# Performance work log

Measured on AMD Instinct MI355X. Metric: run time of the kernel, lower is better.

Reference implementation:

```python
import jax, jax.numpy as jnp
import numpy as np

B, C, H, W = 8, 256, 48, 48


def setup_inputs() -> dict:
    key = jax.random.key(0)
    ks = jax.random.split(key, 16)
    d = {
        "rgb": jax.random.normal(ks[0], (B, C, H, W), dtype=jnp.float32),
        "t": jax.random.normal(ks[1], (B, C, H, W), dtype=jnp.float32),
    }
    names = ["wq1", "bq1", "wk1", "bk1", "wv1", "bv1",
             "wq2", "bq2", "wk2", "bk2", "wv2", "bv2"]
    for i, n in enumerate(names):
        if n.startswith("w"):
            d[n] = jax.random.normal(ks[2 + i], (C, C), dtype=jnp.float32) * 0.02
        else:
            d[n] = jax.random.normal(ks[2 + i], (C,), dtype=jnp.float32) * 0.02
    return d


def _cross_attention(x, y, wq, bq, wk, bk, wv, bv):
    # x, y: [b, c, h, w]; 1x1 convs == channel matmuls (ratio=1)
    b, c, h, w = x.shape
    xf = x.reshape(b, c, h * w)  # [b, c, n]
    yf = y.reshape(b, c, h * w)
    q = jnp.einsum('oi,bin->bno', wq, xf) + bq            # [b, n, c]
    k = jnp.einsum('oi,bin->bon', wk, yf) + bk[None, :, None]  # [b, c, n]
    v = jnp.einsum('oi,bin->bno', wv, yf) + bv            # [b, n, c]
    # unscaled attention, exactly as the torch module (no 1/sqrt(c))
    attn = jax.nn.softmax(jnp.einsum('bnc,bcm->bnm', q, k), axis=-1)  # [b, n, n]
    feat = q + jnp.einsum('bnm,bmc->bnc', attn, v)        # residual on q
    return feat.transpose(0, 2, 1).reshape(b, c, h, w)


def reference(rgb, t, wq1, bq1, wk1, bk1, wv1, bv1,
              wq2, bq2, wk2, bk2, wv2, bv2):
    feat_1 = _cross_attention(rgb, t, wq1, bq1, wk1, bk1, wv1, bv1)
    feat_2 = _cross_attention(t, rgb, wq2, bq2, wk2, bk2, wv2, bv2)
    out1 = rgb + feat_1
    out2 = t + feat_2
    return (out1, out2)
```

## Files before the change

kernel.cpp:

```cpp
#include <hip/hip_runtime.h>
#include <hip/hip_bf16.h>
#include <cstdint>

#define B_ 8
#define C_ 256
#define N_ 2304
#define XT_BYTES ((size_t)B_ * N_ * C_ * 2)
#define QK_BYTES ((size_t)16 * N_ * C_ * 2)
#define V_BYTES  ((size_t)16 * C_ * N_ * 2)

typedef __bf16 bf16x8 __attribute__((ext_vector_type(8)));
typedef float  f32x4  __attribute__((ext_vector_type(4)));
static_assert(sizeof(bf16x8) == 16, "");

__global__ __launch_bounds__(256) void k_transpose(
    const float* __restrict__ rgb, const float* __restrict__ tin,
    char* __restrict__ xT)
{
  const int nt = blockIdx.x;
  const int it = blockIdx.y;
  const int z  = blockIdx.z;
  const int src = z >> 3, b = z & 7;
  const float* __restrict__ in = (src ? tin : rgb) + (size_t)b * C_ * N_;
  char* __restrict__ out = xT + (size_t)src * XT_BYTES + (size_t)b * N_ * 512;
  const int i0 = it * 64, n0 = nt * 64;
  __shared__ float raw[64 * 65];
  const int t = threadIdx.x;
  const int rr = t >> 4;
  const int cc = t & 15;
#pragma unroll
  for (int j = 0; j < 4; ++j) {
    const int ii = rr + 16 * j;
    const float4 v = *(const float4*)(in + (size_t)(i0 + ii) * N_ + n0 + cc * 4);
    float* rp = &raw[ii * 65 + cc * 4];
    rp[0] = v.x; rp[1] = v.y; rp[2] = v.z; rp[3] = v.w;
  }
  __syncthreads();
#pragma unroll
  for (int k = 0; k < 4; ++k) {
    const int nl = rr + 16 * k;
    const int n = n0 + nl;
    union { __bf16 h[4]; uint2 u; } pk;
#pragma unroll
    for (int e = 0; e < 4; ++e)
      pk.h[e] = (__bf16)raw[(cc * 4 + e) * 65 + nl];
    const int cb = ((i0 + cc * 4) * 2) ^ ((n & 7) << 4);
    *(uint2*)(out + (size_t)n * 512 + cb) = pk.u;
  }
}

__global__ __launch_bounds__(256) void k_wcvt(
    const float* __restrict__ w0, const float* __restrict__ w1,
    const float* __restrict__ w2, const float* __restrict__ w3,
    const float* __restrict__ w4, const float* __restrict__ w5,
    char* __restrict__ Wb)
{
  const int widx = blockIdx.y;
  const float* w = widx == 0 ? w0 : widx == 1 ? w1 : widx == 2 ? w2
                 : widx == 3 ? w3 : widx == 4 ? w4 : w5;
  const int t = threadIdx.x;
  const int row = blockIdx.x * 8 + (t >> 5);
  const int c8 = (t & 31) * 8;
  const float4 v0 = *(const float4*)(w + row * 256 + c8);
  const float4 v1 = *(const float4*)(w + row * 256 + c8 + 4);
  union { __bf16 h[8]; uint4 u; } pk;
  pk.h[0] = (__bf16)v0.x; pk.h[1] = (__bf16)v0.y; pk.h[2] = (__bf16)v0.z; pk.h[3] = (__bf16)v0.w;
  pk.h[4] = (__bf16)v1.x; pk.h[5] = (__bf16)v1.y; pk.h[6] = (__bf16)v1.z; pk.h[7] = (__bf16)v1.w;
  const int cb = (c8 * 2) ^ ((row & 7) << 4);
  *(uint4*)(Wb + (size_t)(widx * 256 + row) * 512 + cb) = pk.u;
}

__global__ __launch_bounds__(256, 2) void k_proj_qk(
    const char* __restrict__ xT, const char* __restrict__ Wb,
    const float* __restrict__ bq1, const float* __restrict__ bk1,
    const float* __restrict__ bq2, const float* __restrict__ bk2,
    char* __restrict__ Qw, char* __restrict__ Kw)
{
  const int z = blockIdx.z;
  const int b = blockIdx.y;
  const int ntile = blockIdx.x >> 2, otile = blockIdx.x & 3;
  const int n0 = ntile * 128, o0 = otile * 64;
  const int srcT = (z == 1 || z == 2);
  const char* __restrict__ xp = xT + (size_t)srcT * XT_BYTES + (size_t)b * N_ * 512;
  const char* __restrict__ Wp = Wb + (size_t)z * C_ * 512;
  const float* __restrict__ bias = z == 0 ? bq1 : z == 1 ? bk1 : z == 2 ? bq2 : bk2;
  char* __restrict__ outp = ((z == 0 || z == 2) ? Qw : Kw)
                            + (size_t)((z >= 2 ? 8 : 0) + b) * N_ * 512;

  __shared__ alignas(16) char Alds[128 * 128];
  __shared__ alignas(16) char Wlds[64 * 128];
  const int t = threadIdx.x, lane = t & 63, wid = t >> 6;
  const int wm = wid >> 1, wn = wid & 1;
  const int lr = lane & 15, lk = lane >> 4;
  f32x4 acc[4][2] = {};

  for (int ko = 0; ko < 4; ++ko) {
    const int ib = ko * 128;
    __syncthreads();
#pragma unroll
    for (int s = 0; s < 4; ++s) {
      const int flat = s * 4096 + t * 16;
      *(uint4*)(Alds + flat) =
          *(const uint4*)(xp + (size_t)(n0 + (flat >> 7)) * 512 + ib + (flat & 127));
    }
#pragma unroll
    for (int s = 0; s < 2; ++s) {
      const int flat = s * 4096 + t * 16;
      *(uint4*)(Wlds + flat) =
          *(const uint4*)(Wp + (size_t)(o0 + (flat >> 7)) * 512 + ib + (flat & 127));
    }
    __syncthreads();
#pragma unroll
    for (int ks = 0; ks < 2; ++ks) {
      bf16x8 af[4], bfr[2];
#pragma unroll
      for (int mf = 0; mf < 4; ++mf) {
        const int row = wm * 64 + mf * 16 + lr;
        af[mf] = *(const bf16x8*)(Alds + row * 128 + ((ks * 64 + lk * 16) ^ ((row & 7) << 4)));
      }
#pragma unroll
      for (int nf = 0; nf < 2; ++nf) {
        const int row = wn * 32 + nf * 16 + lr;
        bfr[nf] = *(const bf16x8*)(Wlds + row * 128 + ((ks * 64 + lk * 16) ^ ((row & 7) << 4)));
      }
#pragma unroll
      for (int mf = 0; mf < 4; ++mf)
#pragma unroll
        for (int nf = 0; nf < 2; ++nf)
          acc[mf][nf] = __builtin_amdgcn_mfma_f32_16x16x32_bf16(af[mf], bfr[nf], acc[mf][nf], 0, 0, 0);
    }
  }
#pragma unroll
  for (int nf = 0; nf < 2; ++nf) {
    const int c = o0 + wn * 32 + nf * 16 + lr;
    const float bv = bias[c];
#pragma unroll
    for (int mf = 0; mf < 4; ++mf)
#pragma unroll
      for (int r = 0; r < 4; ++r) {
        const int n = n0 + wm * 64 + mf * 16 + lk * 4 + r;
        *(__bf16*)(outp + (size_t)n * 512 + ((c * 2) ^ ((n & 7) << 4))) =
            (__bf16)(acc[mf][nf][r] + bv);
      }
  }
}

__global__ __launch_bounds__(256, 2) void k_proj_v(
    const char* __restrict__ xT, const char* __restrict__ Wb,
    const float* __restrict__ bv1, const float* __restrict__ bv2,
    char* __restrict__ Vw)
{
  const int z = blockIdx.z;
  const int b = blockIdx.y;
  const int ntile = blockIdx.x >> 2, otile = blockIdx.x & 3;
  const int n0 = ntile * 128, o0 = otile * 64;
  const char* __restrict__ xp = xT + (size_t)(z == 0 ? 1 : 0) * XT_BYTES + (size_t)b * N_ * 512;
  const char* __restrict__ Wp = Wb + (size_t)(4 + z) * C_ * 512;
  const float* __restrict__ bias = z ? bv2 : bv1;
  char* __restrict__ outp = Vw + (size_t)(z * 8 + b) * C_ * 4608;

  __shared__ alignas(16) char Xlds[128 * 128];
  __shared__ alignas(16) char Wlds[64 * 128];
  const int t = threadIdx.x, lane = t & 63, wid = t >> 6;
  const int wm = wid >> 1, wn = wid & 1;
  const int lr = lane & 15, lk = lane >> 4;
  f32x4 acc[2][4] = {};

  for (int ko = 0; ko < 4; ++ko) {
    const int ib = ko * 128;
    __syncthreads();
#pragma unroll
    for (int s = 0; s < 4; ++s) {
      const int flat = s * 4096 + t * 16;
      *(uint4*)(Xlds + flat) =
          *(const uint4*)(xp + (size_t)(n0 + (flat >> 7)) * 512 + ib + (flat & 127));
    }
#pragma unroll
    for (int s = 0; s < 2; ++s) {
      const int flat = s * 4096 + t * 16;
      *(uint4*)(Wlds + flat) =
          *(const uint4*)(Wp + (size_t)(o0 + (flat >> 7)) * 512 + ib + (flat & 127));
    }
    __syncthreads();
#pragma unroll
    for (int ks = 0; ks < 2; ++ks) {
      bf16x8 af[2], bfr[4];
#pragma unroll
      for (int mf = 0; mf < 2; ++mf) {
        const int row = wm * 32 + mf * 16 + lr;
        af[mf] = *(const bf16x8*)(Wlds + row * 128 + ((ks * 64 + lk * 16) ^ ((row & 7) << 4)));
      }
#pragma unroll
      for (int nf = 0; nf < 4; ++nf) {
        const int row = wn * 64 + nf * 16 + lr;
        bfr[nf] = *(const bf16x8*)(Xlds + row * 128 + ((ks * 64 + lk * 16) ^ ((row & 7) << 4)));
      }
#pragma unroll
      for (int mf = 0; mf < 2; ++mf)
#pragma unroll
        for (int nf = 0; nf < 4; ++nf)
          acc[mf][nf] = __builtin_amdgcn_mfma_f32_16x16x32_bf16(af[mf], bfr[nf], acc[mf][nf], 0, 0, 0);
    }
  }
#pragma unroll
  for (int mf = 0; mf < 2; ++mf)
#pragma unroll
    for (int r = 0; r < 4; ++r) {
      const int o = o0 + wm * 32 + mf * 16 + lk * 4 + r;
      const float bv = bias[o];
#pragma unroll
      for (int nf = 0; nf < 4; ++nf) {
        const int n = n0 + wn * 64 + nf * 16 + lr;
        *(__bf16*)(outp + (size_t)o * 4608 + ((n * 2) ^ ((o & 7) << 4))) =
            (__bf16)(acc[mf][nf][r] + bv);
      }
    }
}

__global__ __launch_bounds__(256, 2) void k_flash(
    const char* __restrict__ Qw, const char* __restrict__ Kw, const char* __restrict__ Vw,
    const float* __restrict__ rgb, const float* __restrict__ tin,
    float* __restrict__ outp)
{
  const int qt = blockIdx.x;
  const int pair = blockIdx.y;
  const int a = pair >> 3, b = pair & 7;
  const char* __restrict__ Qp = Qw + (size_t)pair * N_ * 512;
  const char* __restrict__ Kp = Kw + (size_t)pair * N_ * 512;
  const char* __restrict__ Vp = Vw + (size_t)pair * C_ * 4608;
  const float* __restrict__ xsrc = (a ? tin : rgb) + (size_t)b * C_ * N_;
  float* __restrict__ op = outp + (size_t)(a * 8 + b) * C_ * N_;

  __shared__ alignas(16) char Klds[64 * 512];
  __shared__ alignas(16) char Vlds[256 * 128];
  __shared__ alignas(16) char Plds[4 * 2048];

  const int t = threadIdx.x, lane = t & 63, w = t >> 6;
  const int lr = lane & 15, lk = lane >> 4;
  const int q0 = qt * 64;

  bf16x8 qf[8];
  {
    const int n = q0 + w * 16 + lr;
    const char* qrow = Qp + (size_t)n * 512;
    const int sw = (n & 7) << 4;
#pragma unroll
    for (int ks = 0; ks < 8; ++ks)
      qf[ks] = *(const bf16x8*)(qrow + ((ks * 64 + lk * 16) ^ sw));
  }

  f32x4 oacc[16] = {};
  float m_run[4], l_run[4];
#pragma unroll
  for (int r = 0; r < 4; ++r) { m_run[r] = -1e30f; l_run[r] = 0.f; }

  for (int kv = 0; kv < 36; ++kv) {
    const size_t kb = (size_t)kv * 64;
    {
      const char* Ksrc = Kp + kb * 512;
#pragma unroll
      for (int s = 0; s < 8; ++s) {
        const int flat = s * 4096 + t * 16;
        *(uint4*)(Klds + flat) = *(const uint4*)(Ksrc + flat);
      }
      const char* Vsrc = Vp + kb * 2;
#pragma unroll
      for (int s = 0; s < 8; ++s) {
        const int flat = s * 4096 + t * 16;
        *(uint4*)(Vlds + flat) =
            *(const uint4*)(Vsrc + (size_t)(flat >> 7) * 4608 + (flat & 127));
      }
    }
    __syncthreads();

    f32x4 s4[4] = {};
#pragma unroll
    for (int mf = 0; mf < 4; ++mf) {
      const int row = mf * 16 + lr;
      const char* kr = Klds + row * 512;
      const int sw = (row & 7) << 4;
#pragma unroll
      for (int ks = 0; ks < 8; ++ks) {
        const bf16x8 kf = *(const bf16x8*)(kr + ((ks * 64 + lk * 16) ^ sw));
        s4[mf] = __builtin_amdgcn_mfma_f32_16x16x32_bf16(qf[ks], kf, s4[mf], 0, 0, 0);
      }
    }

    float scale[4];
#pragma unroll
    for (int r = 0; r < 4; ++r) {
      float m0 = fmaxf(fmaxf(s4[0][r], s4[1][r]), fmaxf(s4[2][r], s4[3][r]));
      m0 = fmaxf(m0, __shfl_xor(m0, 1));
      m0 = fmaxf(m0, __shfl_xor(m0, 2));
      m0 = fmaxf(m0, __shfl_xor(m0, 4));
      m0 = fmaxf(m0, __shfl_xor(m0, 8));
      const float mn = fmaxf(m_run[r], m0);
      scale[r] = __expf(m_run[r] - mn);
      m_run[r] = mn;
    }

    float psum[4] = {0.f, 0.f, 0.f, 0.f};
    char* pw = Plds + w * 2048;
#pragma unroll
    for (int mf = 0; mf < 4; ++mf)
#pragma unroll
      for (int r = 0; r < 4; ++r) {
        const float p = __expf(s4[mf][r] - m_run[r]);
        psum[r] += p;
        const int row = lk * 4 + r;
        const int col = mf * 16 + lr;
        *(__bf16*)(pw + row * 128 + ((col * 2) ^ ((row & 7) << 4))) = (__bf16)p;
      }
#pragma unroll
    for (int r = 0; r < 4; ++r) {
      float s0 = psum[r];
      s0 += __shfl_xor(s0, 1);
      s0 += __shfl_xor(s0, 2);
      s0 += __shfl_xor(s0, 4);
      s0 += __shfl_xor(s0, 8);
      l_run[r] = l_run[r] * scale[r] + s0;
    }
#pragma unroll
    for (int cf = 0; cf < 16; ++cf)
#pragma unroll
      for (int r = 0; r < 4; ++r) oacc[cf][r] *= scale[r];

#pragma unroll
    for (int ks2 = 0; ks2 < 2; ++ks2) {
      const bf16x8 pf =
          *(const bf16x8*)(pw + lr * 128 + ((ks2 * 64 + lk * 16) ^ ((lr & 7) << 4)));
#pragma unroll
      for (int cf = 0; cf < 16; ++cf) {
        const int vr = cf * 16 + lr;
        const bf16x8 vf =
            *(const bf16x8*)(Vlds + vr * 128 + ((ks2 * 64 + lk * 16) ^ ((vr & 7) << 4)));
        oacc[cf] = __builtin_amdgcn_mfma_f32_16x16x32_bf16(pf, vf, oacc[cf], 0, 0, 0);
      }
    }
    __syncthreads();
  }

  float inv[4];
#pragma unroll
  for (int r = 0; r < 4; ++r) inv[r] = 1.0f / l_run[r];
  const int nb = q0 + w * 16 + lk * 4;
#pragma unroll
  for (int cf = 0; cf < 16; ++cf) {
    const int c = cf * 16 + lr;
    const float4 xv = *(const float4*)(xsrc + (size_t)c * N_ + nb);
    float vals[4];
#pragma unroll
    for (int r = 0; r < 4; ++r) {
      const int n = nb + r;
      const float qv =
          (float)(*(const __bf16*)(Qp + (size_t)n * 512 + ((c * 2) ^ ((n & 7) << 4))));
      vals[r] = oacc[cf][r] * inv[r] + qv;
    }
    float4 ov;
    ov.x = vals[0] + xv.x; ov.y = vals[1] + xv.y;
    ov.z = vals[2] + xv.z; ov.w = vals[3] + xv.w;
    *(float4*)(op + (size_t)c * N_ + nb) = ov;
  }
}

extern "C" void kernel_launch(void* const* d_in, const int* in_sizes, int n_in,
                              void* d_out, int out_size, void* d_ws, size_t ws_size,
                              hipStream_t stream) {
  const float* rgb = (const float*)d_in[0];
  const float* tin = (const float*)d_in[1];
  const float* wq1 = (const float*)d_in[2];
  const float* bq1 = (const float*)d_in[3];
  const float* wk1 = (const float*)d_in[4];
  const float* bk1 = (const float*)d_in[5];
  const float* wv1 = (const float*)d_in[6];
  const float* bv1 = (const float*)d_in[7];
  const float* wq2 = (const float*)d_in[8];
  const float* bq2 = (const float*)d_in[9];
  const float* wk2 = (const float*)d_in[10];
  const float* bk2 = (const float*)d_in[11];
  const float* wv2 = (const float*)d_in[12];
  const float* bv2 = (const float*)d_in[13];

  char* ws = (char*)d_ws;
  char* xT = ws;
  char* Qw = ws + 2 * XT_BYTES;
  char* Kw = Qw + QK_BYTES;
  char* Vw = Kw + QK_BYTES;
  char* Wb = Vw + V_BYTES;

  k_transpose<<<dim3(36, 4, 16), 256, 0, stream>>>(rgb, tin, xT);
  k_wcvt<<<dim3(32, 6), 256, 0, stream>>>(wq1, wk1, wq2, wk2, wv1, wv2, Wb);
  k_proj_qk<<<dim3(72, 8, 4), 256, 0, stream>>>(xT, Wb, bq1, bk1, bq2, bk2, Qw, Kw);
  k_proj_v<<<dim3(72, 8, 2), 256, 0, stream>>>(xT, Wb, bv1, bv2, Vw);
  k_flash<<<dim3(36, 16), 256, 0, stream>>>(Qw, Kw, Vw, rgb, tin, (float*)d_out);
}
```

Baseline: 288.5 us.

## Restructure flash kernel: 128-row Q tiles, async LDS loads, lazy softmax rescale

```diff
diff --git a/kernel.cpp b/kernel.cpp
--- a/kernel.cpp
+++ b/kernel.cpp
@@ -12,6 +12,15 @@
 typedef __bf16 bf16x8 __attribute__((ext_vector_type(8)));
 typedef float  f32x4  __attribute__((ext_vector_type(4)));
 static_assert(sizeof(bf16x8) == 16, "");
+
+__device__ __forceinline__ void gload16(const void* g, void* l) {
+  __builtin_amdgcn_global_load_lds(
+      reinterpret_cast<const __attribute__((address_space(1))) uint32_t*>(
+          reinterpret_cast<uintptr_t>(g)),
+      reinterpret_cast<__attribute__((address_space(3))) uint32_t*>(
+          reinterpret_cast<uintptr_t>(l)),
+      16, 0, 0);
+}
 
 __global__ __launch_bounds__(256) void k_transpose(
     const float* __restrict__ rgb, const float* __restrict__ tin,
@@ -212,12 +221,12 @@
       for (int nf = 0; nf < 4; ++nf) {
         const int n = n0 + wn * 64 + nf * 16 + lr;
         *(__bf16*)(outp + (size_t)o * 4608 + ((n * 2) ^ ((o & 7) << 4))) =
-            (__bf16)(acc[mf][nf][r] + bv);
-      }
-    }
-}
-
-__global__ __launch_bounds__(256, 2) void k_flash(
+            (__bf16)(acc[nf == nf ? mf : mf][nf][r] + bv);
+      }
+    }
+}
+
+__global__ __launch_bounds__(256, 2) void k_flash2(
     const char* __restrict__ Qw, const char* __restrict__ Kw, const char* __restrict__ Vw,
     const float* __restrict__ rgb, const float* __restrict__ tin,
     float* __restrict__ outp)
@@ -231,49 +240,47 @@
   const float* __restrict__ xsrc = (a ? tin : rgb) + (size_t)b * C_ * N_;
   float* __restrict__ op = outp + (size_t)(a * 8 + b) * C_ * N_;
 
-  __shared__ alignas(16) char Klds[64 * 512];
-  __shared__ alignas(16) char Vlds[256 * 128];
-  __shared__ alignas(16) char Plds[4 * 2048];
+  __shared__ alignas(16) char smem[81920];
+  char* Klds = smem;
+  char* Vlds = smem + 32768;
+  char* Plds = smem + 65536;
 
   const int t = threadIdx.x, lane = t & 63, w = t >> 6;
   const int lr = lane & 15, lk = lane >> 4;
-  const int q0 = qt * 64;
-
-  bf16x8 qf[8];
-  {
-    const int n = q0 + w * 16 + lr;
+  const int q0 = qt * 128;
+
+  bf16x8 qf[2][8];
+#pragma unroll
+  for (int qs = 0; qs < 2; ++qs) {
+    const int n = q0 + w * 32 + qs * 16 + lr;
     const char* qrow = Qp + (size_t)n * 512;
     const int sw = (n & 7) << 4;
 #pragma unroll
     for (int ks = 0; ks < 8; ++ks)
-      qf[ks] = *(const bf16x8*)(qrow + ((ks * 64 + lk * 16) ^ sw));
-  }
-
-  f32x4 oacc[16] = {};
-  float m_run[4], l_run[4];
-#pragma unroll
-  for (int r = 0; r < 4; ++r) { m_run[r] = -1e30f; l_run[r] = 0.f; }
+      qf[qs][ks] = *(const bf16x8*)(qrow + ((ks * 64 + lk * 16) ^ sw));
+  }
+
+  f32x4 oacc[2][16] = {};
+  float m_run[2][4], l_run[2][4];
+#pragma unroll
+  for (int qs = 0; qs < 2; ++qs)
+#pragma unroll
+    for (int r = 0; r < 4; ++r) { m_run[qs][r] = -1e30f; l_run[qs][r] = 0.f; }
+
+  {
+#pragma unroll
+    for (int s = 0; s < 8; ++s) {
+      const int flat = s * 4096 + t * 16;
+      gload16(Kp + flat, Klds + flat);
+      gload16(Vp + (size_t)(flat >> 7) * 4608 + (flat & 127), Vlds + flat);
+    }
+  }
 
   for (int kv = 0; kv < 36; ++kv) {
-    const size_t kb = (size_t)kv * 64;
-    {
-      const char* Ksrc = Kp + kb * 512;
-#pragma unroll
-      for (int s = 0; s < 8; ++s) {
-        const int flat = s * 4096 + t * 16;
-        *(uint4*)(Klds + flat) = *(const uint4*)(Ksrc + flat);
-      }
-      const char* Vsrc = Vp + kb * 2;
-#pragma unroll
-      for (int s = 0; s < 8; ++s) {
-        const int flat = s * 4096 + t * 16;
-        *(uint4*)(Vlds + flat) =
-            *(const uint4*)(Vsrc + (size_t)(flat >> 7) * 4608 + (flat & 127));
-      }
-    }
-    __syncthreads();
-
-    f32x4 s4[4] = {};
+    __syncthreads();
+
+    f32x4 s4[2][4] = {};
+    __builtin_amdgcn_s_setprio(1);
 #pragma unroll
     for (int mf = 0; mf < 4; ++mf) {
       const int row = mf * 16 + lr;
@@ -282,84 +289,147 @@
 #pragma unroll
       for (int ks = 0; ks < 8; ++ks) {
         const bf16x8 kf = *(const bf16x8*)(kr + ((ks * 64 + lk * 16) ^ sw));
-        s4[mf] = __builtin_amdgcn_mfma_f32_16x16x32_bf16(qf[ks], kf, s4[mf], 0, 0, 0);
-      }
-    }
-
-    float scale[4];
-#pragma unroll
-    for (int r = 0; r < 4; ++r) {
-      float m0 = fmaxf(fmaxf(s4[0][r], s4[1][r]), fmaxf(s4[2][r], s4[3][r]));
-      m0 = fmaxf(m0, __shfl_xor(m0, 1));
-      m0 = fmaxf(m0, __shfl_xor(m0, 2));
-      m0 = fmaxf(m0, __shfl_xor(m0, 4));
-      m0 = fmaxf(m0, __shfl_xor(m0, 8));
-      const float mn = fmaxf(m_run[r], m0);
-      scale[r] = __expf(m_run[r] - mn);
-      m_run[r] = mn;
-    }
-
-    float psum[4] = {0.f, 0.f, 0.f, 0.f};
-    char* pw = Plds + w * 2048;
-#pragma unroll
-    for (int mf = 0; mf < 4; ++mf)
+        s4[0][mf] = __builtin_amdgcn_mfma_f32_16x16x32_bf16(qf[0][ks], kf, s4[0][mf], 0, 0, 0);
+        s4[1][mf] = __builtin_amdgcn_mfma_f32_16x16x32_bf16(qf[1][ks], kf, s4[1][mf], 0, 0, 0);
+      }
+    }
+    __builtin_amdgcn_s_setprio(0);
+    __syncthreads();
+    if (kv + 1 < 36) {
+      const char* Ksrc = Kp + (size_t)(kv + 1) * 64 * 512;
+#pragma unroll
+      for (int s = 0; s < 8; ++s) {
+        const int flat = s * 4096 + t * 16;
+        gload16(Ksrc + flat, Klds + flat);
+      }
+    }
+
+    float pmax[2][4];
+#pragma unroll
+    for (int qs = 0; qs < 2; ++qs)
 #pragma unroll
       for (int r = 0; r < 4; ++r) {
-        const float p = __expf(s4[mf][r] - m_run[r]);
-        psum[r] += p;
-        const int row = lk * 4 + r;
-        const int col = mf * 16 + lr;
-        *(__bf16*)(pw + row * 128 + ((col * 2) ^ ((row & 7) << 4))) = (__bf16)p;
-      }
-#pragma unroll
-    for (int r = 0; r < 4; ++r) {
-      float s0 = psum[r];
-      s0 += __shfl_xor(s0, 1);
-      s0 += __shfl_xor(s0, 2);
-      s0 += __shfl_xor(s0, 4);
-      s0 += __shfl_xor(s0, 8);
-      l_run[r] = l_run[r] * scale[r] + s0;
-    }
-#pragma unroll
-    for (int cf = 0; cf < 16; ++cf)
-#pragma unroll
-      for (int r = 0; r < 4; ++r) oacc[cf][r] *= scale[r];
-
+        float m0 = fmaxf(fmaxf(s4[qs][0][r], s4[qs][1][r]),
+                         fmaxf(s4[qs][2][r], s4[qs][3][r]));
+        m0 = fmaxf(m0, __shfl_xor(m0, 1));
+        m0 = fmaxf(m0, __shfl_xor(m0, 2));
+        m0 = fmaxf(m0, __shfl_xor(m0, 4));
+        m0 = fmaxf(m0, __shfl_xor(m0, 8));
+        pmax[qs][r] = m0;
+      }
+    bool need = false;
+#pragma unroll
+    for (int qs = 0; qs < 2; ++qs)
+#pragma unroll
+      for (int r = 0; r < 4; ++r)
+        need |= (pmax[qs][r] > m_run[qs][r] + 8.f);
+    if (__any(need)) {
+#pragma unroll
+      for (int qs = 0; qs < 2; ++qs)
+#pragma unroll
+        for (int r = 0; r < 4; ++r) {
+          const float mn = fmaxf(m_run[qs][r], pmax[qs][r]);
+          const float sc = __expf(m_run[qs][r] - mn);
+          m_run[qs][r] = mn;
+          l_run[qs][r] *= sc;
+#pragma unroll
+          for (int cf = 0; cf < 16; ++cf) oacc[qs][cf][r] *= sc;
+        }
+    }
+
+    char* pw = Plds + w * 4096;
+#pragma unroll
+    for (int qs = 0; qs < 2; ++qs) {
+      float psum[4] = {0.f, 0.f, 0.f, 0.f};
+#pragma unroll
+      for (int mf = 0; mf < 4; ++mf)
+#pragma unroll
+        for (int r = 0; r < 4; ++r) {
+          const float p = __expf(s4[qs][mf][r] - m_run[qs][r]);
+          psum[r] += p;
+          const int row = qs * 16 + lk * 4 + r;
+          const int col = mf * 16 + lr;
+          *(__bf16*)(pw + row * 128 + ((col * 2) ^ ((row & 7) << 4))) = (__bf16)p;
+        }
+#pragma unroll
+      for (int r = 0; r < 4; ++r) {
+        float s0 = psum[r];
+        s0 += __shfl_xor(s0, 1);
+        s0 += __shfl_xor(s0, 2);
+        s0 += __shfl_xor(s0, 4);
+        s0 += __shfl_xor(s0, 8);
+        l_run[qs][r] += s0;
+      }
+    }
+
+    __builtin_amdgcn_s_setprio(1);
 #pragma unroll
     for (int ks2 = 0; ks2 < 2; ++ks2) {
-      const bf16x8 pf =
-          *(const bf16x8*)(pw + lr * 128 + ((ks2 * 64 + lk * 16) ^ ((lr & 7) << 4)));
+      bf16x8 pf[2];
+#pragma unroll
+      for (int qs = 0; qs < 2; ++qs) {
+        const int prow = qs * 16 + lr;
+        pf[qs] = *(const bf16x8*)(pw + prow * 128 +
+                                  ((ks2 * 64 + lk * 16) ^ ((prow & 7) << 4)));
+      }
 #pragma unroll
       for (int cf = 0; cf < 16; ++cf) {
         const int vr = cf * 16 + lr;
         const bf16x8 vf =
             *(const bf16x8*)(Vlds + vr * 128 + ((ks2 * 64 + lk * 16) ^ ((vr & 7) << 4)));
-        oacc[cf] = __builtin_amdgcn_mfma_f32_16x16x32_bf16(pf, vf, oacc[cf], 0, 0, 0);
-      }
-    }
-    __syncthreads();
-  }
-
-  float inv[4];
-#pragma unroll
-  for (int r = 0; r < 4; ++r) inv[r] = 1.0f / l_run[r];
-  const int nb = q0 + w * 16 + lk * 4;
-#pragma unroll
-  for (int cf = 0; cf < 16; ++cf) {
-    const int c = cf * 16 + lr;
-    const float4 xv = *(const float4*)(xsrc + (size_t)c * N_ + nb);
-    float vals[4];
-#pragma unroll
-    for (int r = 0; r < 4; ++r) {
-      const int n = nb + r;
-      const float qv =
-          (float)(*(const __bf16*)(Qp + (size_t)n * 512 + ((c * 2) ^ ((n & 7) << 4))));
-      vals[r] = oacc[cf][r] * inv[r] + qv;
-    }
-    float4 ov;
-    ov.x = vals[0] + xv.x; ov.y = vals[1] + xv.y;
-    ov.z = vals[2] + xv.z; ov.w = vals[3] + xv.w;
-    *(float4*)(op + (size_t)c * N_ + nb) = ov;
+        oacc[0][cf] = __builtin_amdgcn_mfma_f32_16x16x32_bf16(pf[0], vf, oacc[0][cf], 0, 0, 0);
+        oacc[1][cf] = __builtin_amdgcn_mfma_f32_16x16x32_bf16(pf[1], vf, oacc[1][cf], 0, 0, 0);
+      }
+    }
+    __builtin_amdgcn_s_setprio(0);
+    __syncthreads();
+    if (kv + 1 < 36) {
+      const char* Vsrc = Vp + (size_t)(kv + 1) * 128;
+#pragma unroll
+      for (int s = 0; s < 8; ++s) {
+        const int flat = s * 4096 + t * 16;
+        gload16(Vsrc + (size_t)(flat >> 7) * 4608 + (flat & 127), Vlds + flat);
+      }
+    }
+  }
+
+  {
+    const char* Qsrc = Qp + (size_t)q0 * 512;
+#pragma unroll
+    for (int s = 0; s < 16; ++s) {
+      const int flat = s * 4096 + t * 16;
+      gload16(Qsrc + flat, smem + flat);
+    }
+  }
+  __syncthreads();
+
+  float inv[2][4];
+#pragma unroll
+  for (int qs = 0; qs < 2; ++qs)
+#pragma unroll
+    for (int r = 0; r < 4; ++r) inv[qs][r] = 1.0f / l_run[qs][r];
+
+#pragma unroll
+  for (int qs = 0; qs < 2; ++qs) {
+    const int nb = q0 + w * 32 + qs * 16 + lk * 4;
+    const int nl0 = w * 32 + qs * 16 + lk * 4;
+#pragma unroll
+    for (int cf = 0; cf < 16; ++cf) {
+      const int c = cf * 16 + lr;
+      const float4 xv = *(const float4*)(xsrc + (size_t)c * N_ + nb);
+      float vals[4];
+#pragma unroll
+      for (int r = 0; r < 4; ++r) {
+        const int nl = nl0 + r;
+        const float qv =
+            (float)(*(const __bf16*)(smem + (size_t)nl * 512 + ((c * 2) ^ ((nl & 7) << 4))));
+        vals[r] = oacc[qs][cf][r] * inv[qs][r] + qv;
+      }
+      float4 ov;
+      ov.x = vals[0] + xv.x; ov.y = vals[1] + xv.y;
+      ov.z = vals[2] + xv.z; ov.w = vals[3] + xv.w;
+      *(float4*)(op + (size_t)c * N_ + nb) = ov;
+    }
   }
 }
 
@@ -392,5 +462,5 @@
   k_wcvt<<<dim3(32, 6), 256, 0, stream>>>(wq1, wk1, wq2, wk2, wv1, wv2, Wb);
   k_proj_qk<<<dim3(72, 8, 4), 256, 0, stream>>>(xT, Wb, bq1, bk1, bq2, bk2, Qw, Kw);
   k_proj_v<<<dim3(72, 8, 2), 256, 0, stream>>>(xT, Wb, bv1, bv2, Vw);
-  k_flash<<<dim3(36, 16), 256, 0, stream>>>(Qw, Kw, Vw, rgb, tin, (float*)d_out);
-}
+  k_flash2<<<dim3(18, 16), 256, 0, stream>>>(Qw, Kw, Vw, rgb, tin, (float*)d_out);
+}
```

New measurement: 659.2 us. 2.28x slower.

## Stream K via async LDS loads, read V from global, lazy softmax rescale

Applied to the files above, without the earlier changes.

```diff
diff --git a/kernel.cpp b/kernel.cpp
--- a/kernel.cpp
+++ b/kernel.cpp
@@ -12,6 +12,15 @@
 typedef __bf16 bf16x8 __attribute__((ext_vector_type(8)));
 typedef float  f32x4  __attribute__((ext_vector_type(4)));
 static_assert(sizeof(bf16x8) == 16, "");
+
+__device__ __forceinline__ void gload16(const void* g, void* l) {
+  __builtin_amdgcn_global_load_lds(
+      reinterpret_cast<const __attribute__((address_space(1))) uint32_t*>(
+          reinterpret_cast<uintptr_t>(g)),
+      reinterpret_cast<__attribute__((address_space(3))) uint32_t*>(
+          reinterpret_cast<uintptr_t>(l)),
+      16, 0, 0);
+}
 
 __global__ __launch_bounds__(256) void k_transpose(
     const float* __restrict__ rgb, const float* __restrict__ tin,
@@ -211,13 +220,13 @@
 #pragma unroll
       for (int nf = 0; nf < 4; ++nf) {
         const int n = n0 + wn * 64 + nf * 16 + lr;
-        *(__bf16*)(outp + (size_t)o * 4608 + ((n * 2) ^ ((o & 7) << 4))) =
+        *(__bf16*)(outp + (size_t)o * 4608 + n * 2) =
             (__bf16)(acc[mf][nf][r] + bv);
       }
     }
 }
 
-__global__ __launch_bounds__(256, 2) void k_flash(
+__global__ __launch_bounds__(256, 3) void k_flash3(
     const char* __restrict__ Qw, const char* __restrict__ Kw, const char* __restrict__ Vw,
     const float* __restrict__ rgb, const float* __restrict__ tin,
     float* __restrict__ outp)
@@ -231,9 +240,9 @@
   const float* __restrict__ xsrc = (a ? tin : rgb) + (size_t)b * C_ * N_;
   float* __restrict__ op = outp + (size_t)(a * 8 + b) * C_ * N_;
 
-  __shared__ alignas(16) char Klds[64 * 512];
-  __shared__ alignas(16) char Vlds[256 * 128];
-  __shared__ alignas(16) char Plds[4 * 2048];
+  __shared__ alignas(16) char smem[40960];
+  char* Klds = smem;
+  char* Plds = smem + 32768;
 
   const int t = threadIdx.x, lane = t & 63, w = t >> 6;
   const int lr = lane & 15, lk = lane >> 4;
@@ -249,31 +258,24 @@
       qf[ks] = *(const bf16x8*)(qrow + ((ks * 64 + lk * 16) ^ sw));
   }
 
+  const char* vbase = Vp + (size_t)lr * 4608 + lk * 16;
+
   f32x4 oacc[16] = {};
   float m_run[4], l_run[4];
 #pragma unroll
   for (int r = 0; r < 4; ++r) { m_run[r] = -1e30f; l_run[r] = 0.f; }
 
+#pragma unroll
+  for (int s = 0; s < 8; ++s) {
+    const int flat = s * 4096 + t * 16;
+    gload16(Kp + flat, Klds + flat);
+  }
+
   for (int kv = 0; kv < 36; ++kv) {
-    const size_t kb = (size_t)kv * 64;
-    {
-      const char* Ksrc = Kp + kb * 512;
-#pragma unroll
-      for (int s = 0; s < 8; ++s) {
-        const int flat = s * 4096 + t * 16;
-        *(uint4*)(Klds + flat) = *(const uint4*)(Ksrc + flat);
-      }
-      const char* Vsrc = Vp + kb * 2;
-#pragma unroll
-      for (int s = 0; s < 8; ++s) {
-        const int flat = s * 4096 + t * 16;
-        *(uint4*)(Vlds + flat) =
-            *(const uint4*)(Vsrc + (size_t)(flat >> 7) * 4608 + (flat & 127));
-      }
-    }
     __syncthreads();
 
     f32x4 s4[4] = {};
+    __builtin_amdgcn_s_setprio(1);
 #pragma unroll
     for (int mf = 0; mf < 4; ++mf) {
       const int row = mf * 16 + lr;
@@ -285,8 +287,18 @@
         s4[mf] = __builtin_amdgcn_mfma_f32_16x16x32_bf16(qf[ks], kf, s4[mf], 0, 0, 0);
       }
     }
-
-    float scale[4];
+    __builtin_amdgcn_s_setprio(0);
+    __syncthreads();
+    if (kv + 1 < 36) {
+      const char* Ksrc = Kp + (size_t)(kv + 1) * 64 * 512;
+#pragma unroll
+      for (int s = 0; s < 8; ++s) {
+        const int flat = s * 4096 + t * 16;
+        gload16(Ksrc + flat, Klds + flat);
+      }
+    }
+
+    float pmax[4];
 #pragma unroll
     for (int r = 0; r < 4; ++r) {
       float m0 = fmaxf(fmaxf(s4[0][r], s4[1][r]), fmaxf(s4[2][r], s4[3][r]));
@@ -294,56 +306,79 @@
       m0 = fmaxf(m0, __shfl_xor(m0, 2));
       m0 = fmaxf(m0, __shfl_xor(m0, 4));
       m0 = fmaxf(m0, __shfl_xor(m0, 8));
-      const float mn = fmaxf(m_run[r], m0);
-      scale[r] = __expf(m_run[r] - mn);
-      m_run[r] = mn;
-    }
-
-    float psum[4] = {0.f, 0.f, 0.f, 0.f};
+      pmax[r] = m0;
+    }
+    bool need = false;
+#pragma unroll
+    for (int r = 0; r < 4; ++r) need |= (pmax[r] > m_run[r] + 8.f);
+    if (__any(need)) {
+#pragma unroll
+      for (int r = 0; r < 4; ++r) {
+        const float mn = fmaxf(m_run[r], pmax[r]);
+        const float sc = __expf(m_run[r] - mn);
+        m_run[r] = mn;
+        l_run[r] *= sc;
+#pragma unroll
+        for (int cf = 0; cf < 16; ++cf) oacc[cf][r] *= sc;
+      }
+    }
+
     char* pw = Plds + w * 2048;
-#pragma unroll
-    for (int mf = 0; mf < 4; ++mf)
+    {
+      float psum[4] = {0.f, 0.f, 0.f, 0.f};
+#pragma unroll
+      for (int mf = 0; mf < 4; ++mf)
+#pragma unroll
+        for (int r = 0; r < 4; ++r) {
+          const float p = __expf(s4[mf][r] - m_run[r]);
+          psum[r] += p;
+          const int row = lk * 4 + r;
+          const int col = mf * 16 + lr;
+          *(__bf16*)(pw + row * 128 + ((col * 2) ^ ((row & 7) << 4))) = (__bf16)p;
+        }
 #pragma unroll
       for (int r = 0; r < 4; ++r) {
-        const float p = __expf(s4[mf][r] - m_run[r]);
-        psum[r] += p;
-        const int row = lk * 4 + r;
-        const int col = mf * 16 + lr;
-        *(__bf16*)(pw + row * 128 + ((col * 2) ^ ((row & 7) << 4))) = (__bf16)p;
-      }
-#pragma unroll
-    for (int r = 0; r < 4; ++r) {
-      float s0 = psum[r];
-      s0 += __shfl_xor(s0, 1);
-      s0 += __shfl_xor(s0, 2);
-      s0 += __shfl_xor(s0, 4);
-      s0 += __shfl_xor(s0, 8);
-      l_run[r] = l_run[r] * scale[r] + s0;
-    }
-#pragma unroll
-    for (int cf = 0; cf < 16; ++cf)
-#pragma unroll
-      for (int r = 0; r < 4; ++r) oacc[cf][r] *= scale[r];
-
+        float s0 = psum[r];
+        s0 += __shfl_xor(s0, 1);
+        s0 += __shfl_xor(s0, 2);
+        s0 += __shfl_xor(s0, 4);
+        s0 += __shfl_xor(s0, 8);
+        l_run[r] += s0;
+      }
+    }
+
+    const char* vkv = vbase + (size_t)kv * 128;
+    __builtin_amdgcn_s_setprio(1);
 #pragma unroll
     for (int ks2 = 0; ks2 < 2; ++ks2) {
       const bf16x8 pf =
           *(const bf16x8*)(pw + lr * 128 + ((ks2 * 64 + lk * 16) ^ ((lr & 7) << 4)));
+      const char* vk = vkv + ks2 * 64;
 #pragma unroll
       for (int cf = 0; cf < 16; ++cf) {
-        const int vr = cf * 16 + lr;
-        const bf16x8 vf =
-            *(const bf16x8*)(Vlds + vr * 128 + ((ks2 * 64 + lk * 16) ^ ((vr & 7) << 4)));
+        const bf16x8 vf = *(const bf16x8*)(vk + (size_t)cf * 16 * 4608);
         oacc[cf] = __builtin_amdgcn_mfma_f32_16x16x32_bf16(pf, vf, oacc[cf], 0, 0, 0);
       }
     }
-    __syncthreads();
-  }
+    __builtin_amdgcn_s_setprio(0);
+  }
+
+  __syncthreads();
+  {
+    const char* Qsrc = Qp + (size_t)q0 * 512;
+#pragma unroll
+    for (int s = 0; s < 8; ++s) {
+      const int flat = s * 4096 + t * 16;
+      gload16(Qsrc + flat, Klds + flat);
+    }
+  }
+  __syncthreads();
 
   float inv[4];
 #pragma unroll
   for (int r = 0; r < 4; ++r) inv[r] = 1.0f / l_run[r];
   const int nb = q0 + w * 16 + lk * 4;
+  const int nl0 = w * 16 + lk * 4;
 #pragma unroll
   for (int cf = 0; cf < 16; ++cf) {
     const int c = cf * 16 + lr;
@@ -351,9 +386,9 @@
     float vals[4];
 #pragma unroll
     for (int r = 0; r < 4; ++r) {
-      const int n = nb + r;
+      const int nl = nl0 + r;
       const float qv =
-          (float)(*(const __bf16*)(Qp + (size_t)n * 512 + ((c * 2) ^ ((n & 7) << 4))));
+          (float)(*(const __bf16*)(Klds + (size_t)nl * 512 + ((c * 2) ^ ((nl & 7) << 4))));
       vals[r] = oacc[cf][r] * inv[r] + qv;
     }
     float4 ov;
@@ -392,5 +427,5 @@
   k_wcvt<<<dim3(32, 6), 256, 0, stream>>>(wq1, wk1, wq2, wk2, wv1, wv2, Wb);
   k_proj_qk<<<dim3(72, 8, 4), 256, 0, stream>>>(xT, Wb, bq1, bk1, bq2, bk2, Qw, Kw);
   k_proj_v<<<dim3(72, 8, 2), 256, 0, stream>>>(xT, Wb, bv1, bv2, Vw);
-  k_flash<<<dim3(36, 16), 256, 0, stream>>>(Qw, Kw, Vw, rgb, tin, (float*)d_out);
-}
+  k_flash3<<<dim3(36, 16), 256, 0, stream>>>(Qw, Kw, Vw, rgb, tin, (float*)d_out);
+}
```

Measured after the change: 641.0 us. 2.22x slower.
